# Performance work log

Hardware: AMD Instinct MI355X
Metric: run time of the kernel (lower is better)

Reference implementation:

```python
import jax, jax.numpy as jnp
import numpy as np

DIM = 2048
HEADS = 16
HEAD_DIM = DIM // HEADS
B, S = 2, 2048


def setup_inputs() -> dict:
    key = jax.random.key(0)
    k1, k2, k3 = jax.random.split(key, 3)
    x = jax.random.normal(k1, (B, S, DIM), dtype=jnp.float32)
    # causal mask (True = keep), realistic production usage of masked_fill(mask==0,...)
    mask = jnp.tril(jnp.ones((S, S), dtype=bool))
    scale = 1.0 / np.sqrt(DIM)
    W_qkv = jax.random.normal(k2, (DIM, 3 * DIM), dtype=jnp.float32) * scale
    b_qkv = jnp.zeros((3 * DIM,), dtype=jnp.float32)
    W_out = jax.random.normal(k3, (DIM, DIM), dtype=jnp.float32) * scale
    b_out = jnp.zeros((DIM,), dtype=jnp.float32)
    return {"x": x, "mask": mask, "W_qkv": W_qkv, "b_qkv": b_qkv,
            "W_out": W_out, "b_out": b_out}


def reference(x, mask, W_qkv, b_qkv, W_out, b_out):
    b, s, d = x.shape
    # fused QKV projection: [b,s,3d]
    qkv = jnp.einsum('bsd,de->bse', x, W_qkv) + b_qkv
    # [b, s, h, 3*hd] -> [b, h, s, 3*hd] -> chunk into q,k,v
    qkv = qkv.reshape(b, s, HEADS, 3 * HEAD_DIM).transpose(0, 2, 1, 3)
    q, k, v = jnp.split(qkv, 3, axis=-1)  # each [b,h,s,hd]
    scores = jnp.einsum('bhqd,bhkd->bhqk', q, k) / np.sqrt(HEAD_DIM)
    scores = jnp.where(mask, scores, jnp.float32(-1e9))
    attn = jax.nn.softmax(scores, axis=-1)
    # dropout_rate = 0.0 (eval) -> identity
    out = jnp.einsum('bhqk,bhkd->bhqd', attn, v)  # [b,h,s,hd]
    out = out.transpose(0, 2, 1, 3).reshape(b, s, d)
    return jnp.einsum('bsd,de->bse', out, W_out) + b_out
```

## Files before the change

kernel.cpp:

```cpp
#include <hip/hip_runtime.h>
#include <hip/hip_bf16.h>

#define SEQ   2048
#define DIMSZ 2048
#define NHEAD 16
#define HD    128
#define KDIM  2048

typedef __attribute__((ext_vector_type(8))) short bf16x8;
typedef __attribute__((ext_vector_type(4))) float f32x4;
typedef __attribute__((ext_vector_type(4))) short short4v;
typedef __attribute__((ext_vector_type(4))) float float4v;

__device__ __forceinline__ short f2bf(float f) {
    union { __hip_bfloat16 h; short s; } u;
    u.h = __float2bfloat16(f);
    return u.s;
}

__device__ __forceinline__ unsigned pack_bf2(float lo, float hi) {
    return (unsigned)(unsigned short)f2bf(lo) | ((unsigned)(unsigned short)f2bf(hi) << 16);
}

__device__ __forceinline__ void gload_lds16(const void* g, void* l) {
    __builtin_amdgcn_global_load_lds(
        (const __attribute__((address_space(1))) void*)g,
        (__attribute__((address_space(3))) void*)l, 16, 0, 0);
}

__global__ __launch_bounds__(256) void fused_prep(const float* __restrict__ x,
                                                  short* __restrict__ x_bf,
                                                  const float* __restrict__ W_qkv,
                                                  short* __restrict__ wqkv_t,
                                                  const float* __restrict__ W_out,
                                                  short* __restrict__ wout_t) {
    __shared__ float tile[32][33];
    const int bid = blockIdx.x, tid = threadIdx.x;
    if (bid < 8192) {
        int i = (bid * 256 + tid) * 4;
        float4v v = *reinterpret_cast<const float4v*>(x + i);
        short4v o;
        o[0] = f2bf(v[0]); o[1] = f2bf(v[1]); o[2] = f2bf(v[2]); o[3] = f2bf(v[3]);
        *reinterpret_cast<short4v*>(x_bf + i) = o;
        return;
    }
    const float* in;
    short* out;
    int R, C, c0, r0;
    if (bid < 20480) {
        int tb = bid - 8192;
        in = W_qkv; out = wqkv_t; R = 2048; C = 6144;
        c0 = (tb % 192) * 32; r0 = (tb / 192) * 32;
    } else {
        int tb = bid - 20480;
        in = W_out; out = wout_t; R = 2048; C = 2048;
        c0 = (tb % 64) * 32; r0 = (tb / 64) * 32;
    }
    const int tx = tid & 31, ty = tid >> 5;
#pragma unroll
    for (int i = 0; i < 32; i += 8)
        tile[ty + i][tx] = in[(long)(r0 + ty + i) * C + c0 + tx];
    __syncthreads();
#pragma unroll
    for (int i = 0; i < 32; i += 8)
        out[(long)(c0 + ty + i) * R + r0 + tx] = f2bf(tile[tx][ty + i]);
}

template <int MODE, int BM, int BN, int WMC, int WNC>
__global__ __launch_bounds__(512, 2) void gemm8p(const short* __restrict__ A,
                                                 const short* __restrict__ Bt,
                                                 const float* __restrict__ bias,
                                                 float* __restrict__ outf,
                                                 short* __restrict__ q_buf,
                                                 short* __restrict__ k_buf,
                                                 short* __restrict__ vt_buf,
                                                 int ntx) {
    constexpr int QMW = (BM / 2) / WMC;
    constexpr int QNW = (BN / 2) / WNC;
    constexpr int MA = QMW / 16;
    constexpr int NB = QNW / 16;
    constexpr int UA = BM / 64, UB = BN / 64, UT = UA + UB;
    constexpr int RA = MA * 2, RB = NB * 2;
    constexpr int BH0C = (BN / 2 + 63) / 64;
    constexpr int NE = UA / 2 + BH0C, NL = UT - NE;
    constexpr int S0 = 2, S2 = 2;
    constexpr int VM0 = NE + S0;
    constexpr int VM2 = NL + S2;
    constexpr int VM3 = (NE - S2) + NE;
    constexpr int NT = KDIM / 64;

    __shared__ __align__(16) short Alds[2][BM * 64];
    __shared__ __align__(16) short Blds[2][BN * 64];

    const int tid = threadIdx.x;
    const int wv = tid >> 6, ln = tid & 63;
    const int lr = ln & 15, lg = ln >> 4;
    const int wm = wv / WNC, wn = wv % WNC;
    const int q8 = gridDim.x >> 3;
    const int id = blockIdx.x;
    const int swz = (id & 7) * q8 + (id >> 3);
    const int m0 = (swz / ntx) * BM, n0 = (swz % ntx) * BN;

    const int r_l = wv * 8 + (ln >> 3);
    const int g8 = ((ln & 7) ^ ((ln >> 3) & 7)) << 3;

#define STAGE_U(u, bufi, TT)                                                   \
    {                                                                          \
        const bool isA_ = (u) < UA / 2 || (u) >= UA / 2 + UB;                  \
        const int idx_ = (u) < UA / 2 ? (u)                                    \
                         : ((u) < UA / 2 + UB ? (u) - UA / 2 : (u) - UB);      \
        if (isA_)                                                              \
            gload_lds16(A + (long)(m0 + idx_ * 64 + r_l) * KDIM + (TT)*64 + g8,\
                        &Alds[bufi][idx_ * 4096 + wv * 512]);                  \
        else                                                                   \
            gload_lds16(Bt + (long)(n0 + idx_ * 64 + r_l) * KDIM + (TT)*64 + g8,\
                        &Blds[bufi][idx_ * 4096 + wv * 512]);                  \
    }

#define RD(L_, row_, kk_) \
    (*reinterpret_cast<const bf16x8*>(&(L_)[(row_)*64 + ((((kk_)*4 + lg) ^ ((row_)&7)) << 3)]))

#define RD_A(bufi, mh, bank)                                                   \
    _Pragma("unroll") for (int mi = 0; mi < MA; ++mi) {                        \
        int r_ = (mh) * (BM / 2) + wm * QMW + mi * 16 + lr;                    \
        bank[mi][0] = RD(Alds[bufi], r_, 0);                                   \
        bank[mi][1] = RD(Alds[bufi], r_, 1);                                   \
    }
#define RD_B(bufi, nh, bank)                                                   \
    _Pragma("unroll") for (int ni = 0; ni < NB; ++ni) {                        \
        int r_ = (nh) * (BN / 2) + wn * QNW + ni * 16 + lr;                    \
        bank[ni][0] = RD(Blds[bufi], r_, 0);                                   \
        bank[ni][1] = RD(Blds[bufi], r_, 1);                                   \
    }

#define MFMA_Q(qi, AB, BB)                                                     \
    __builtin_amdgcn_s_setprio(1);                                             \
    _Pragma("unroll") for (int kk = 0; kk < 2; ++kk)                           \
        _Pragma("unroll") for (int mi = 0; mi < MA; ++mi)                      \
            _Pragma("unroll") for (int ni = 0; ni < NB; ++ni)                  \
                acc[qi][mi][ni] = __builtin_amdgcn_mfma_f32_16x16x32_bf16(     \
                    AB[mi][kk], BB[ni][kk], acc[qi][mi][ni], 0, 0, 0);         \
    __builtin_amdgcn_s_setprio(0);

#define LGKM(n)                                                                \
    asm volatile("s_waitcnt lgkmcnt(%0)" ::"i"(n) : "memory");                 \
    __builtin_amdgcn_sched_barrier(0);
#define VMC(n) asm volatile("s_waitcnt vmcnt(%0)" ::"i"(n) : "memory");
#define BAR()                                                                  \
    __builtin_amdgcn_s_barrier();                                              \
    __builtin_amdgcn_sched_barrier(0);

    f32x4 acc[4][MA][NB] = {};
    bf16x8 aF0[MA][2], aF1[MA][2], bF0a[NB][2], bF0b[NB][2], bF1[NB][2];

#pragma unroll
    for (int u = 0; u < UT; ++u) STAGE_U(u, 0, 0);
#pragma unroll
    for (int u = 0; u < NE; ++u) STAGE_U(u, 1, 1);
    VMC(NE);
    BAR();
    RD_A(0, 0, aF0);
    RD_B(0, 0, bF0a);

#define TILE_BODY(PAR, T_, BF0C, BF0N)                                         \
    {                                                                          \
        constexpr int cur = PAR, nxt = PAR ^ 1;                                \
        RD_B(cur, 1, bF1);                                                     \
        if ((T_) + 1 < NT) {                                                   \
            STAGE_U(NE + 0, nxt, (T_) + 1);                                    \
            STAGE_U(NE + 1, nxt, (T_) + 1);                                    \
        }                                                                      \
        LGKM(RB);                                                              \
        MFMA_Q(0, aF0, BF0C);                                                  \
        VMC(VM0);                                                              \
        BAR();                                                                 \
        RD_A(cur, 1, aF1);                                                     \
        if ((T_) + 1 < NT) {                                                   \
            _Pragma("unroll") for (int u = NE + S0; u < UT; ++u)               \
                STAGE_U(u, nxt, (T_) + 1);                                     \
        }                                                                      \
        LGKM(RA);                                                              \
        MFMA_Q(1, aF0, bF1);                                                   \
        BAR();                                                                 \
        if ((T_) + 2 < NT) {                                                   \
            STAGE_U(0, cur, (T_) + 2);                                         \
            STAGE_U(1, cur, (T_) + 2);                                         \
        }                                                                      \
        LGKM(0);                                                               \
        MFMA_Q(2, aF1, bF1);                                                   \
        if ((T_) + 2 < NT) { VMC(VM2); } else { VMC(NL); }                     \
        BAR();                                                                 \
        if ((T_) + 1 < NT) {                                                   \
            RD_A(nxt, 0, aF0);                                                 \
            RD_B(nxt, 0, BF0N);                                                \
        }                                                                      \
        if ((T_) + 2 < NT) {                                                   \
            _Pragma("unroll") for (int u = S2; u < NE; ++u)                    \
                STAGE_U(u, cur, (T_) + 2);                                     \
        }                                                                      \
        LGKM(RA + RB);                                                         \
        MFMA_Q(3, aF1, BF0C);                                                  \
        if ((T_) + 2 < NT) { VMC(VM3); } else { VMC(0); }                      \
        BAR();                                                                 \
    }

    for (int TT = 0; TT < NT; TT += 2) {
        TILE_BODY(0, TT, bF0a, bF0b);
        TILE_BODY(1, TT + 1, bF0b, bF0a);
    }

    const int MH[4] = {0, 0, 1, 1}, NHq[4] = {0, 1, 1, 0};
#pragma unroll
    for (int q = 0; q < 4; ++q) {
#pragma unroll
        for (int mi = 0; mi < MA; ++mi) {
#pragma unroll
            for (int ni = 0; ni < NB; ++ni) {
                int col = n0 + NHq[q] * (BN / 2) + wn * QNW + ni * 16 + lr;
                float bv = bias[col];
#pragma unroll
                for (int j = 0; j < 4; ++j) {
                    int row = m0 + MH[q] * (BM / 2) + wm * QMW + mi * 16 + lg * 4 + j;
                    float v = acc[q][mi][ni][j] + bv;
                    if (MODE == 0) {
                        int h = col / (3 * HD);
                        int jj = col - h * (3 * HD);
                        int b = row >> 11, s = row & 2047;
                        int bh = b * NHEAD + h;
                        short sv = f2bf(v);
                        if (jj < HD)
                            q_buf[(bh * SEQ + s) * HD + jj] = sv;
                        else if (jj < 2 * HD)
                            k_buf[(bh * SEQ + s) * HD + (jj - HD)] = sv;
                        else
                            vt_buf[(bh * HD + (jj - 2 * HD)) * SEQ + s] = sv;
                    } else {
                        outf[(long)row * DIMSZ + col] = v;
                    }
                }
            }
        }
    }
#undef STAGE_U
#undef RD
#undef RD_A
#undef RD_B
#undef MFMA_Q
#undef LGKM
#undef VMC
#undef BAR
#undef TILE_BODY
}

__global__ __launch_bounds__(256, 2) void attn_kernel(const short* __restrict__ q_buf,
                                                      const short* __restrict__ k_buf,
                                                      const short* __restrict__ vt_buf,
                                                      short* __restrict__ ao) {
    __shared__ __align__(16) short Klds[2][64 * 128];
    __shared__ __align__(16) short Vlds[2][128 * 64];
    const int tid = threadIdx.x;
    const int wave = tid >> 6, lane = tid & 63;
    const int lr = lane & 15, lg = lane >> 4;
    const int bx = blockIdx.x;
    const int qt = 15 - (bx >> 5);
    const int bh = bx & 31;
    const int b = bh >> 4, h = bh & 15;
    const int qbase = qt * 128 + wave * 32;
    const float c2 = 0.12752775f;

    bf16x8 qf[2][4];
    {
        const short* qrow = q_buf + ((long)(bh * SEQ + qbase + lr)) * HD;
#pragma unroll
        for (int mi = 0; mi < 2; ++mi)
#pragma unroll
            for (int c = 0; c < 4; ++c)
                qf[mi][c] = *reinterpret_cast<const bf16x8*>(
                    qrow + mi * 16 * HD + c * 32 + lg * 8);
    }
    asm volatile("s_waitcnt vmcnt(0)" ::: "memory");

    const char* kbase = (const char*)(k_buf + (long)bh * SEQ * HD);
    const char* vbase = (const char*)(vt_buf + (long)bh * HD * SEQ);
    const int krow_l = wave * 4 + (lane >> 4);
    const int kcol_l = ((lane & 15) * 16) ^ ((krow_l & 7) << 4);
    const int vrow_l = wave * 8 + (lane >> 3);
    const int vcol_l = ((lane & 7) * 16) ^ ((vrow_l & 7) << 4);

    const int nt = 2 * (qt + 1);
    auto stage = [&](int bufi, int t) {
        const char* ks = kbase + (long)t * 16384 + (long)krow_l * 256 + kcol_l;
        const char* vs = vbase + (long)t * 128 + (long)vrow_l * (SEQ * 2) + vcol_l;
        short* kd = &Klds[bufi][wave * 512];
        short* vd = &Vlds[bufi][wave * 512];
#pragma unroll
        for (int i = 0; i < 4; ++i) {
            gload_lds16(ks + i * 4096, kd + i * 2048);
            gload_lds16(vs + (long)i * 32 * SEQ * 2, vd + i * 2048);
        }
    };

    f32x4 o_acc[2][8] = {};
    float mrow[2] = {-1e30f, -1e30f}, lrow[2] = {0.f, 0.f};

    const int s0 = (lane & 15) | ((lane & 16) << 1);
    const int s1 = s0 + 16;
    const bool hi_ni = (lane & 32) != 0;

    stage(0, 0);
    for (int t = 0; t < nt; ++t) {
        const int cur = t & 1;
        if (t + 1 < nt) {
            stage(cur ^ 1, t + 1);
            asm volatile("s_waitcnt vmcnt(8)" ::: "memory");
        } else {
            asm volatile("s_waitcnt vmcnt(0)" ::: "memory");
        }
        __builtin_amdgcn_s_barrier();
        __builtin_amdgcn_sched_barrier(0);

        const int kv0 = t * 64;
        if (kv0 <= qbase + 31) {
            const short* kl = &Klds[cur][0];
            const short* vl = &Vlds[cur][0];
            bf16x8 kf[4][4];
#pragma unroll
            for (int c = 0; c < 4; ++c)
#pragma unroll
                for (int ni = 0; ni < 4; ++ni)
                    kf[c][ni] = *reinterpret_cast<const bf16x8*>(
                        kl + (((ni * 16 + lr) * 256 +
                               ((c * 64 + lg * 16) ^ ((lr & 7) << 4))) >> 1));
            f32x4 sc[2][4] = {};
            __builtin_amdgcn_s_setprio(1);
#pragma unroll
            for (int c = 0; c < 4; ++c)
#pragma unroll
                for (int mi = 0; mi < 2; ++mi)
#pragma unroll
                    for (int ni = 0; ni < 4; ++ni)
                        sc[mi][ni] = __builtin_amdgcn_mfma_f32_16x16x32_bf16(
                            kf[c][ni], qf[mi][c], sc[mi][ni], 0, 0, 0);
            __builtin_amdgcn_s_setprio(0);
            bf16x8 vfr[2][8];
#pragma unroll
            for (int kc = 0; kc < 2; ++kc)
#pragma unroll
                for (int n = 0; n < 8; ++n)
                    vfr[kc][n] = *reinterpret_cast<const bf16x8*>(
                        vl + (((n * 16 + lr) * 128 +
                               ((kc * 64 + lg * 16) ^ ((lr & 7) << 4))) >> 1));
            const bool full = (kv0 + 63) <= qbase;
            float mx[2];
#pragma unroll
            for (int mi = 0; mi < 2; ++mi) {
                float m_ = -3e38f;
                const int qg = qbase + mi * 16 + lr;
#pragma unroll
                for (int ni = 0; ni < 4; ++ni)
#pragma unroll
                    for (int j = 0; j < 4; ++j) {
                        float v = sc[mi][ni][j] * c2;
                        if (!full && (kv0 + ni * 16 + lg * 4 + j > qg)) v = -1e9f;
                        sc[mi][ni][j] = v;
                        m_ = fmaxf(m_, v);
                    }
                mx[mi] = m_;
            }
#pragma unroll
            for (int mi = 0; mi < 2; ++mi) {
                mx[mi] = fmaxf(mx[mi], __shfl_xor(mx[mi], 16, 64));
                mx[mi] = fmaxf(mx[mi], __shfl_xor(mx[mi], 32, 64));
            }
            float md = fmaxf(mx[0] - mrow[0], mx[1] - mrow[1]);
            if (!__all(md <= 11.5f)) {
#pragma unroll
                for (int mi = 0; mi < 2; ++mi) {
                    float mn = fmaxf(mrow[mi], mx[mi]);
                    float a = exp2f(mrow[mi] - mn);
                    mrow[mi] = mn;
                    lrow[mi] *= a;
#pragma unroll
                    for (int j = 0; j < 4; ++j) {
                        float aj = __shfl(a, (lane & 48) | (lg * 4 + j), 64);
#pragma unroll
                        for (int n = 0; n < 8; ++n)
                            o_acc[mi][n][j] *= aj;
                    }
                }
            }
            unsigned pk[2][4][2];
#pragma unroll
            for (int mi = 0; mi < 2; ++mi) {
                float ps = 0.f;
#pragma unroll
                for (int ni = 0; ni < 4; ++ni) {
#pragma unroll
                    for (int j = 0; j < 4; ++j) {
                        float p = exp2f(sc[mi][ni][j] - mrow[mi]);
                        sc[mi][ni][j] = p;
                        ps += p;
                    }
                    pk[mi][ni][0] = pack_bf2(sc[mi][ni][0], sc[mi][ni][1]);
                    pk[mi][ni][1] = pack_bf2(sc[mi][ni][2], sc[mi][ni][3]);
                }
                lrow[mi] += ps;
            }
#pragma unroll
            for (int kc = 0; kc < 2; ++kc) {
                union { int i[4]; bf16x8 v; } pa[2];
#pragma unroll
                for (int mi = 0; mi < 2; ++mi) {
                    int a0 = __shfl((int)pk[mi][2 * kc][0], s0, 64);
                    int b0 = __shfl((int)pk[mi][2 * kc + 1][0], s0, 64);
                    int a1 = __shfl((int)pk[mi][2 * kc][1], s0, 64);
                    int b1 = __shfl((int)pk[mi][2 * kc + 1][1], s0, 64);
                    int a2 = __shfl((int)pk[mi][2 * kc][0], s1, 64);
                    int b2 = __shfl((int)pk[mi][2 * kc + 1][0], s1, 64);
                    int a3 = __shfl((int)pk[mi][2 * kc][1], s1, 64);
                    int b3 = __shfl((int)pk[mi][2 * kc + 1][1], s1, 64);
                    pa[mi].i[0] = hi_ni ? b0 : a0;
                    pa[mi].i[1] = hi_ni ? b1 : a1;
                    pa[mi].i[2] = hi_ni ? b2 : a2;
                    pa[mi].i[3] = hi_ni ? b3 : a3;
                }
                __builtin_amdgcn_s_setprio(1);
#pragma unroll
                for (int n = 0; n < 8; ++n)
#pragma unroll
                    for (int mi = 0; mi < 2; ++mi)
                        o_acc[mi][n] = __builtin_amdgcn_mfma_f32_16x16x32_bf16(
                            pa[mi].v, vfr[kc][n], o_acc[mi][n], 0, 0, 0);
                __builtin_amdgcn_s_setprio(0);
            }
        }
        __builtin_amdgcn_s_barrier();
    }

    float invq[2];
#pragma unroll
    for (int mi = 0; mi < 2; ++mi) {
        float s = lrow[mi];
        s += __shfl_xor(s, 16, 64);
        s += __shfl_xor(s, 32, 64);
        invq[mi] = 1.0f / s;
    }
    short* aor = ao + ((long)(b * SEQ + qbase) * DIMSZ + h * HD);
#pragma unroll
    for (int mi = 0; mi < 2; ++mi)
#pragma unroll
        for (int j = 0; j < 4; ++j) {
            float ij = __shfl(invq[mi], (lane & 48) | (lg * 4 + j), 64);
#pragma unroll
            for (int n = 0; n < 8; ++n)
                aor[(mi * 16 + lg * 4 + j) * DIMSZ + n * 16 + lr] =
                    f2bf(o_acc[mi][n][j] * ij);
        }
}

extern "C" void kernel_launch(void* const* d_in, const int* in_sizes, int n_in,
                              void* d_out, int out_size, void* d_ws, size_t ws_size,
                              hipStream_t stream) {
    const float* x     = (const float*)d_in[0];
    const float* W_qkv = (const float*)d_in[2];
    const float* b_qkv = (const float*)d_in[3];
    const float* W_out = (const float*)d_in[4];
    const float* b_out = (const float*)d_in[5];
    float* out = (float*)d_out;

    char* ws = (char*)d_ws;
    short* x_bf   = (short*)ws;
    short* wqkv_t = (short*)(ws + (size_t)16 * 1048576);
    short* wout_t = (short*)(ws + (size_t)40 * 1048576);
    short* q_buf  = (short*)(ws + (size_t)48 * 1048576);
    short* k_buf  = (short*)(ws + (size_t)64 * 1048576);
    short* vt_buf = (short*)(ws + (size_t)80 * 1048576);
    short* ao     = x_bf;

    fused_prep<<<24576, 256, 0, stream>>>(x, x_bf, W_qkv, wqkv_t, W_out, wout_t);
    gemm8p<0, 256, 192, 4, 2><<<512, 512, 0, stream>>>(x_bf, wqkv_t, b_qkv, nullptr,
                                                       q_buf, k_buf, vt_buf, 32);
    attn_kernel<<<512, 256, 0, stream>>>(q_buf, k_buf, vt_buf, ao);
    gemm8p<1, 128, 256, 2, 4><<<256, 512, 0, stream>>>(ao, wout_t, b_out, out,
                                                       nullptr, nullptr, nullptr, 8);
}
```

Baseline: 288.6 us.

## Single-buffer V tile and interleave K/V staging to raise attention occupancy

The attention kernel drops double buffering for V, so LDS use falls from 64KB to 48KB, and launch bounds rise to 3 blocks per SM. V for tile t is now loaded during QK^T and softmax of the same tile, and K for t+1 is prefetched after the QK MFMAs. K and V fragments are read from LDS just before use rather than all up front, which lowers register pressure. This adds a second barrier and a full vmcnt(0) wait per iteration, which may expose load latency. The extra waves per CU are meant to hide that latency.

```diff
diff --git a/kernel.cpp b/kernel.cpp
--- a/kernel.cpp
+++ b/kernel.cpp
@@ -252,12 +252,12 @@
 #undef TILE_BODY
 }
 
-__global__ __launch_bounds__(256, 2) void attn_kernel(const short* __restrict__ q_buf,
+__global__ __launch_bounds__(256, 3) void attn_kernel(const short* __restrict__ q_buf,
                                                       const short* __restrict__ k_buf,
                                                       const short* __restrict__ vt_buf,
                                                       short* __restrict__ ao) {
     __shared__ __align__(16) short Klds[2][64 * 128];
-    __shared__ __align__(16) short Vlds[2][128 * 64];
+    __shared__ __align__(16) short Vlds[128 * 64];
     const int tid = threadIdx.x;
     const int wave = tid >> 6, lane = tid & 63;
     const int lr = lane & 15, lg = lane >> 4;
@@ -288,16 +288,19 @@
     const int vcol_l = ((lane & 7) * 16) ^ ((vrow_l & 7) << 4);
 
     const int nt = 2 * (qt + 1);
-    auto stage = [&](int bufi, int t) {
+    auto stageK = [&](int bufi, int t) {
         const char* ks = kbase + (long)t * 16384 + (long)krow_l * 256 + kcol_l;
+        short* kd = &Klds[bufi][wave * 512];
+#pragma unroll
+        for (int i = 0; i < 4; ++i)
+            gload_lds16(ks + i * 4096, kd + i * 2048);
+    };
+    auto stageV = [&](int t) {
         const char* vs = vbase + (long)t * 128 + (long)vrow_l * (SEQ * 2) + vcol_l;
-        short* kd = &Klds[bufi][wave * 512];
-        short* vd = &Vlds[bufi][wave * 512];
-#pragma unroll
-        for (int i = 0; i < 4; ++i) {
-            gload_lds16(ks + i * 4096, kd + i * 2048);
+        short* vd = &Vlds[wave * 512];
+#pragma unroll
+        for (int i = 0; i < 4; ++i)
             gload_lds16(vs + (long)i * 32 * SEQ * 2, vd + i * 2048);
-        }
     };
 
     f32x4 o_acc[2][8] = {};
@@ -307,49 +310,43 @@
     const int s1 = s0 + 16;
     const bool hi_ni = (lane & 32) != 0;
 
-    stage(0, 0);
+    stageK(0, 0);
+    asm volatile("s_waitcnt vmcnt(0)" ::: "memory");
+    __builtin_amdgcn_s_barrier();
+    __builtin_amdgcn_sched_barrier(0);
+
     for (int t = 0; t < nt; ++t) {
         const int cur = t & 1;
-        if (t + 1 < nt) {
-            stage(cur ^ 1, t + 1);
-            asm volatile("s_waitcnt vmcnt(8)" ::: "memory");
-        } else {
-            asm volatile("s_waitcnt vmcnt(0)" ::: "memory");
-        }
-        __builtin_amdgcn_s_barrier();
-        __builtin_amdgcn_sched_barrier(0);
-
         const int kv0 = t * 64;
-        if (kv0 <= qbase + 31) {
+        const bool work = kv0 <= qbase + 31;
+
+        stageV(t);
+
+        f32x4 sc[2][4] = {};
+        if (work) {
             const short* kl = &Klds[cur][0];
-            const short* vl = &Vlds[cur][0];
-            bf16x8 kf[4][4];
-#pragma unroll
-            for (int c = 0; c < 4; ++c)
+#pragma unroll
+            for (int c = 0; c < 4; ++c) {
+                bf16x8 kf[4];
 #pragma unroll
                 for (int ni = 0; ni < 4; ++ni)
-                    kf[c][ni] = *reinterpret_cast<const bf16x8*>(
+                    kf[ni] = *reinterpret_cast<const bf16x8*>(
                         kl + (((ni * 16 + lr) * 256 +
                                ((c * 64 + lg * 16) ^ ((lr & 7) << 4))) >> 1));
-            f32x4 sc[2][4] = {};
-            __builtin_amdgcn_s_setprio(1);
-#pragma unroll
-            for (int c = 0; c < 4; ++c)
+                __builtin_amdgcn_s_setprio(1);
 #pragma unroll
                 for (int mi = 0; mi < 2; ++mi)
 #pragma unroll
                     for (int ni = 0; ni < 4; ++ni)
                         sc[mi][ni] = __builtin_amdgcn_mfma_f32_16x16x32_bf16(
-                            kf[c][ni], qf[mi][c], sc[mi][ni], 0, 0, 0);
-            __builtin_amdgcn_s_setprio(0);
-            bf16x8 vfr[2][8];
-#pragma unroll
-            for (int kc = 0; kc < 2; ++kc)
-#pragma unroll
-                for (int n = 0; n < 8; ++n)
-                    vfr[kc][n] = *reinterpret_cast<const bf16x8*>(
-                        vl + (((n * 16 + lr) * 128 +
-                               ((kc * 64 + lg * 16) ^ ((lr & 7) << 4))) >> 1));
+                            kf[ni], qf[mi][c], sc[mi][ni], 0, 0, 0);
+                __builtin_amdgcn_s_setprio(0);
+            }
+        }
+        if (t + 1 < nt) stageK(cur ^ 1, t + 1);
+
+        unsigned pk[2][4][2];
+        if (work) {
             const bool full = (kv0 + 63) <= qbase;
             float mx[2];
 #pragma unroll
@@ -389,7 +386,6 @@
                     }
                 }
             }
-            unsigned pk[2][4][2];
 #pragma unroll
             for (int mi = 0; mi < 2; ++mi) {
                 float ps = 0.f;
@@ -406,6 +402,18 @@
                 }
                 lrow[mi] += ps;
             }
+        }
+
+        if (t + 1 < nt) {
+            asm volatile("s_waitcnt vmcnt(4)" ::: "memory");
+        } else {
+            asm volatile("s_waitcnt vmcnt(0)" ::: "memory");
+        }
+        __builtin_amdgcn_s_barrier();
+        __builtin_amdgcn_sched_barrier(0);
+
+        if (work) {
+            const short* vl = &Vlds[0];
 #pragma unroll
             for (int kc = 0; kc < 2; ++kc) {
                 union { int i[4]; bf16x8 v; } pa[2];
@@ -424,17 +432,24 @@
                     pa[mi].i[2] = hi_ni ? b2 : a2;
                     pa[mi].i[3] = hi_ni ? b3 : a3;
                 }
-                __builtin_amdgcn_s_setprio(1);
-#pragma unroll
-                for (int n = 0; n < 8; ++n)
+#pragma unroll
+                for (int n = 0; n < 8; ++n) {
+                    bf16x8 vf = *reinterpret_cast<const bf16x8*>(
+                        vl + (((n * 16 + lr) * 128 +
+                               ((kc * 64 + lg * 16) ^ ((lr & 7) << 4))) >> 1));
+                    __builtin_amdgcn_s_setprio(1);
 #pragma unroll
                     for (int mi = 0; mi < 2; ++mi)
                         o_acc[mi][n] = __builtin_amdgcn_mfma_f32_16x16x32_bf16(
-                            pa[mi].v, vfr[kc][n], o_acc[mi][n], 0, 0, 0);
-                __builtin_amdgcn_s_setprio(0);
+                            pa[mi].v, vf, o_acc[mi][n], 0, 0, 0);
+                    __builtin_amdgcn_s_setprio(0);
+                }
             }
         }
+
+        asm volatile("s_waitcnt vmcnt(0)" ::: "memory");
         __builtin_amdgcn_s_barrier();
+        __builtin_amdgcn_sched_barrier(0);
     }
 
     float invq[2];
```

Result: slower. 331.5 us (+14.9%).
